# Optimization experiments

Hardware: AMD Instinct MI355X
Metric: run time of the kernel (lower is better)

Reference implementation:

```python
import jax, jax.numpy as jnp
import numpy as np

D_C = 16  # c // 4 with c = 64
BN_EPS = 1e-5


def _block(x, w, b, g, beta, m, v, a):
    """Conv2Dblock with 1x1 conv: pointwise conv -> BatchNorm2d (inference) -> PReLU."""
    y = jnp.einsum('oi,bift->boft', w, x) + b[None, :, None, None]
    scale = (g / jnp.sqrt(v + BN_EPS))[None, :, None, None]
    y = (y - m[None, :, None, None]) * scale + beta[None, :, None, None]
    return jnp.where(y >= 0, y, a * y)  # PReLU, single shared slope


def _asa(inp, fqkv, tqk, proj):
    b, c, f, t = inp.shape
    scale = 1.0 / np.sqrt(D_C)
    neg = -jnp.finfo(inp.dtype).max

    # frequency attention
    f_qkv = _block(inp, *fqkv)                      # [b, 3*d_c interleaved, f, t]
    f_qkv = f_qkv.reshape(b, D_C, 3, f, t)          # '(c k)' split, k fastest
    qf, kf, v = f_qkv[:, :, 0], f_qkv[:, :, 1], f_qkv[:, :, 2]
    f_score = jnp.einsum('bcft,bcyt->btfy', qf, kf) * scale
    f_score = jax.nn.softmax(f_score, axis=-1)
    f_out = jnp.einsum('btfy,bcyt->bcft', f_score, v)

    # causal time attention
    t_qk = _block(inp, *tqk)                        # [b, 2*d_c interleaved, f, t]
    t_qk = t_qk.reshape(b, D_C, 2, f, t)
    qt, kt = t_qk[:, :, 0], t_qk[:, :, 1]
    t_score = jnp.einsum('bcft,bcfy->bfty', qt, kt) * scale
    causal_mask = jnp.triu(jnp.ones((t, t), dtype=bool), 1)  # strictly upper => future
    t_score = jnp.where(causal_mask[None, None], neg, t_score)
    t_score = jax.nn.softmax(t_score, axis=-1)
    t_out = jnp.einsum('bfty,bcfy->bcft', t_score, f_out)

    out = _block(t_out, *proj)
    return out + inp


def setup_inputs() -> dict:
    key = jax.random.key(0)
    ks = jax.random.split(key, 24)
    B, C, F, T = 2, 64, 257, 500
    dc = D_C

    def conv_params(ki, kb, out_ch, in_ch):
        w = jax.random.normal(ki, (out_ch, in_ch), jnp.float32) * (1.0 / np.sqrt(in_ch))
        b = jax.random.normal(kb, (out_ch,), jnp.float32) * 0.02
        return w, b

    inp = jax.random.normal(ks[0], (B, C, F, T), jnp.float32)

    fqkv_w, fqkv_b = conv_params(ks[1], ks[2], 3 * dc, C)
    fqkv_g = 1.0 + 0.1 * jax.random.uniform(ks[3], (3 * dc,), jnp.float32)
    fqkv_beta = 0.02 * jax.random.normal(ks[4], (3 * dc,), jnp.float32)
    fqkv_m = 0.02 * jax.random.normal(ks[5], (3 * dc,), jnp.float32)
    fqkv_v = 0.9 + 0.2 * jax.random.uniform(ks[6], (3 * dc,), jnp.float32)
    fqkv_a = jnp.full((1,), 0.25, jnp.float32)

    tqk_w, tqk_b = conv_params(ks[7], ks[8], 2 * dc, C)
    tqk_g = 1.0 + 0.1 * jax.random.uniform(ks[9], (2 * dc,), jnp.float32)
    tqk_beta = 0.02 * jax.random.normal(ks[10], (2 * dc,), jnp.float32)
    tqk_m = 0.02 * jax.random.normal(ks[11], (2 * dc,), jnp.float32)
    tqk_v = 0.9 + 0.2 * jax.random.uniform(ks[12], (2 * dc,), jnp.float32)
    tqk_a = jnp.full((1,), 0.25, jnp.float32)

    proj_w, proj_b = conv_params(ks[13], ks[14], C, dc)
    proj_g = 1.0 + 0.1 * jax.random.uniform(ks[15], (C,), jnp.float32)
    proj_beta = 0.02 * jax.random.normal(ks[16], (C,), jnp.float32)
    proj_m = 0.02 * jax.random.normal(ks[17], (C,), jnp.float32)
    proj_v = 0.9 + 0.2 * jax.random.uniform(ks[18], (C,), jnp.float32)
    proj_a = jnp.full((1,), 0.25, jnp.float32)

    return dict(inp=inp,
                fqkv_w=fqkv_w, fqkv_b=fqkv_b, fqkv_g=fqkv_g, fqkv_beta=fqkv_beta,
                fqkv_m=fqkv_m, fqkv_v=fqkv_v, fqkv_a=fqkv_a,
                tqk_w=tqk_w, tqk_b=tqk_b, tqk_g=tqk_g, tqk_beta=tqk_beta,
                tqk_m=tqk_m, tqk_v=tqk_v, tqk_a=tqk_a,
                proj_w=proj_w, proj_b=proj_b, proj_g=proj_g, proj_beta=proj_beta,
                proj_m=proj_m, proj_v=proj_v, proj_a=proj_a)


def reference(inp, fqkv_w, fqkv_b, fqkv_g, fqkv_beta, fqkv_m, fqkv_v, fqkv_a,
              tqk_w, tqk_b, tqk_g, tqk_beta, tqk_m, tqk_v, tqk_a,
              proj_w, proj_b, proj_g, proj_beta, proj_m, proj_v, proj_a):
    return _asa(inp,
                (fqkv_w, fqkv_b, fqkv_g, fqkv_beta, fqkv_m, fqkv_v, fqkv_a),
                (tqk_w, tqk_b, tqk_g, tqk_beta, tqk_m, tqk_v, tqk_a),
                (proj_w, proj_b, proj_g, proj_beta, proj_m, proj_v, proj_a))
```

## Files before the change

kernel.cpp:

```cpp
#include <hip/hip_runtime.h>

#define BB 2
#define CIN 64
#define FD 257
#define TD 500
#define FT (FD*TD)
#define EPS 1e-5f
#define NEGINF (-3.0e38f)
#define FDP 260
#define FDP4 260
#define FQT_PLANE (TD*FDP)
#define LOG2E 1.44269504088896f
#define EXP2F(x) __builtin_amdgcn_exp2f(x)

typedef _Float16 half_t;
typedef half_t half2_t __attribute__((ext_vector_type(2)));
typedef half_t half4 __attribute__((ext_vector_type(4)));
typedef float  f32x4 __attribute__((ext_vector_type(4)));

__global__ __launch_bounds__(256) void stage1_kernel(
    const float* __restrict__ x,
    const float* __restrict__ fw, const float* __restrict__ fb_,
    const float* __restrict__ fg, const float* __restrict__ fbe,
    const float* __restrict__ fm, const float* __restrict__ fv_,
    const float* __restrict__ fa,
    const float* __restrict__ tw, const float* __restrict__ tb_,
    const float* __restrict__ tg, const float* __restrict__ tbe,
    const float* __restrict__ tm, const float* __restrict__ tv_,
    const float* __restrict__ ta,
    half_t* __restrict__ fq, half_t* __restrict__ tq)
{
    __shared__ float Wl[80*64];
    __shared__ float Bl[80];
    const int tid = threadIdx.x;
    for (int idx = tid; idx < 80*64; idx += 256) {
        const int o = idx >> 6, i = idx & 63;
        float sc, wv;
        if (o < 48) { sc = fg[o]*rsqrtf(fv_[o]+EPS); wv = fw[o*64+i]; }
        else { const int o2 = o-48; sc = tg[o2]*rsqrtf(tv_[o2]+EPS); wv = tw[o2*64+i]; }
        Wl[idx] = wv*sc;
    }
    if (tid < 80) {
        const int o = tid;
        if (o < 48) Bl[o] = (fb_[o]-fm[o])*(fg[o]*rsqrtf(fv_[o]+EPS)) + fbe[o];
        else { const int o2 = o-48; Bl[o] = (tb_[o2]-tm[o2])*(tg[o2]*rsqrtf(tv_[o2]+EPS)) + tbe[o2]; }
    }
    __syncthreads();
    const float af = fa[0], at = ta[0];
    const int og = tid >> 6, lane = tid & 63;
    const int b  = blockIdx.x / 1004;
    const int nb = blockIdx.x % 1004;
    const long n0 = (long)nb*128 + lane*2;
    if (n0 >= FT) return;

    float2 acc[20];
    #pragma unroll
    for (int j = 0; j < 20; ++j) {
        const float bv = Bl[og*20+j];
        acc[j] = make_float2(bv, bv);
    }
    const float* xb = x + (long)b*CIN*FT + n0;
    #pragma unroll 2
    for (int i = 0; i < 64; i += 4) {
        const float* xi = xb + (long)i*FT;
        const float2 a0 = *(const float2*)(xi);
        const float2 a1 = *(const float2*)(xi + FT);
        const float2 a2 = *(const float2*)(xi + 2*FT);
        const float2 a3 = *(const float2*)(xi + 3*FT);
        #pragma unroll
        for (int j = 0; j < 20; ++j) {
            const float4 wv = *(const float4*)&Wl[(og*20+j)*64 + i];
            acc[j].x += wv.x*a0.x + wv.y*a1.x + wv.z*a2.x + wv.w*a3.x;
            acc[j].y += wv.x*a0.y + wv.y*a1.y + wv.z*a2.y + wv.w*a3.y;
        }
    }
    #pragma unroll
    for (int j = 0; j < 20; ++j) {
        const int o = og*20 + j;
        const float a_ = (o < 48) ? af : at;
        float vx = acc[j].x, vy = acc[j].y;
        vx = vx >= 0.f ? vx : a_*vx;
        vy = vy >= 0.f ? vy : a_*vy;
        half2_t hv; hv[0] = (half_t)vx; hv[1] = (half_t)vy;
        half_t* dst = (o < 48) ? (fq + ((long)b*48 + o)*FT + n0)
                               : (tq + ((long)b*32 + (o-48))*FT + n0);
        *(half2_t*)dst = hv;
    }
}

__global__ __launch_bounds__(256) void transpose_h2h_kernel(
    const half_t* __restrict__ src, half_t* __restrict__ dst,
    int R, int C, int RP)
{
    __shared__ half_t tile[64][68];
    const int plane = blockIdx.x;
    const int rb = blockIdx.y*64, cb = blockIdx.z*64;
    const half_t* s = src + (long)plane*R*C;
    half_t* d = dst + (long)plane*C*RP;
    const int q4 = (threadIdx.x & 15)*4;
    const int wl = threadIdx.x >> 4;
    #pragma unroll
    for (int p = 0; p < 4; ++p) {
        const int r = rb + wl + 16*p;
        const int c = cb + q4;
        half4 v = {(half_t)0.f,(half_t)0.f,(half_t)0.f,(half_t)0.f};
        if (r < R) {
            const half_t* srow = s + (long)r*C;
            if (c + 3 < C) v = *(const half4*)(srow + c);
            else {
                #pragma unroll
                for (int e = 0; e < 4; ++e) if (c+e < C) v[e] = srow[c+e];
            }
        }
        *(half4*)&tile[wl + 16*p][q4] = v;
    }
    __syncthreads();
    #pragma unroll
    for (int p = 0; p < 4; ++p) {
        const int c = cb + wl + 16*p;
        if (c >= C) continue;
        const int r0 = rb + q4;
        half4 o;
        #pragma unroll
        for (int e = 0; e < 4; ++e) o[e] = tile[q4 + e][wl + 16*p];
        half_t* drow = d + (long)c*RP;
        if (r0 + 3 < RP) *(half4*)(drow + r0) = o;
        else {
            #pragma unroll
            for (int e = 0; e < 4; ++e) if (r0+e < RP) drow[r0+e] = o[e];
        }
    }
}

__global__ __launch_bounds__(256) void transpose_f2h_kernel(
    const float* __restrict__ src, half_t* __restrict__ dst,
    int R, int C, int CS, int RP)
{
    __shared__ half_t tile[64][68];
    const int plane = blockIdx.x;
    const int rb = blockIdx.y*64, cb = blockIdx.z*64;
    const float* s = src + (long)plane*R*CS;
    half_t* d = dst + (long)plane*C*RP;
    const int q4 = (threadIdx.x & 15)*4;
    const int wl = threadIdx.x >> 4;
    #pragma unroll
    for (int p = 0; p < 4; ++p) {
        const int r = rb + wl + 16*p;
        const int c = cb + q4;
        half4 v = {(half_t)0.f,(half_t)0.f,(half_t)0.f,(half_t)0.f};
        if (r < R) {
            const float* srow = s + (long)r*CS;
            if (c + 3 < C) {
                const float4 fv = *(const float4*)(srow + c);
                v[0] = (half_t)fv.x; v[1] = (half_t)fv.y;
                v[2] = (half_t)fv.z; v[3] = (half_t)fv.w;
            } else {
                #pragma unroll
                for (int e = 0; e < 4; ++e) if (c+e < C) v[e] = (half_t)srow[c+e];
            }
        }
        *(half4*)&tile[wl + 16*p][q4] = v;
    }
    __syncthreads();
    #pragma unroll
    for (int p = 0; p < 4; ++p) {
        const int c = cb + wl + 16*p;
        if (c >= C) continue;
        const int r0 = rb + q4;
        half4 o;
        #pragma unroll
        for (int e = 0; e < 4; ++e) o[e] = tile[q4 + e][wl + 16*p];
        half_t* drow = d + (long)c*RP;
        if (r0 + 3 < RP) *(half4*)(drow + r0) = o;
        else {
            #pragma unroll
            for (int e = 0; e < 4; ++e) if (r0+e < RP) drow[r0+e] = o[e];
        }
    }
}

__global__ __launch_bounds__(512) void fattn_kernel(
    const half_t* __restrict__ fqT, float* __restrict__ foT)
{
    __shared__ half_t KT[272*20];
    __shared__ half_t QT[272*20];
    __shared__ half_t Vs[16*280];
    const int tid = threadIdx.x;
    const int b = blockIdx.x / TD, t = blockIdx.x % TD;
    const half_t* base = fqT + (long)b*48*FQT_PLANE + (long)t*FDP;
    const half_t qsc = (half_t)(0.25f*LOG2E);
    for (int s = tid; s < 48*68; s += 512) {
        const int c3 = s / 68, j = s - c3*68;
        const int f0 = 4*j;
        half4 v = {(half_t)0.f,(half_t)0.f,(half_t)0.f,(half_t)0.f};
        if (f0 < FDP) v = *(const half4*)(base + (long)c3*FQT_PLANE + f0);
        const int c = c3 / 3, wh = c3 - 3*c;
        if (wh == 0) {
            #pragma unroll
            for (int e = 0; e < 4; ++e) QT[(f0+e)*20 + c] = v[e]*qsc;
        } else if (wh == 1) {
            #pragma unroll
            for (int e = 0; e < 4; ++e) KT[(f0+e)*20 + c] = v[e];
        } else {
            *(half4*)&Vs[c*280 + f0] = v;
        }
    }
    __syncthreads();
    const int w = tid >> 6, lane = tid & 63;
    const int lmod = lane & 15, ldiv = lane >> 4;
    for (int ft = w; ft < 17; ft += 8) {
        const int f0 = 16*ft;
        const half4 qb = *(const half4*)&QT[(f0+lmod)*20 + 4*ldiv];
        f32x4 o = {0.f,0.f,0.f,0.f};
        float m = NEGINF, l = 0.f;
        for (int yt = 0; yt < 16; yt += 2) {
            const int y0 = 16*yt;
            const half4 ka0 = *(const half4*)&KT[(y0   +lmod)*20 + 4*ldiv];
            const half4 ka1 = *(const half4*)&KT[(y0+16+lmod)*20 + 4*ldiv];
            f32x4 s0 = __builtin_amdgcn_mfma_f32_16x16x16f16(
                ka0, qb, (f32x4){0.f,0.f,0.f,0.f}, 0, 0, 0);
            f32x4 s1 = __builtin_amdgcn_mfma_f32_16x16x16f16(
                ka1, qb, (f32x4){0.f,0.f,0.f,0.f}, 0, 0, 0);
            float mt = fmaxf(fmaxf(fmaxf(s0[0],s0[1]), fmaxf(s0[2],s0[3])),
                             fmaxf(fmaxf(s1[0],s1[1]), fmaxf(s1[2],s1[3])));
            mt = fmaxf(mt, __shfl_xor(mt, 16, 64));
            mt = fmaxf(mt, __shfl_xor(mt, 32, 64));
            const float mn = fmaxf(m, mt);
            const float alpha = EXP2F(m - mn);
            half4 pb0, pb1; float ps = 0.f;
            #pragma unroll
            for (int r = 0; r < 4; ++r) {
                const float p0 = EXP2F(s0[r] - mn);
                const float p1 = EXP2F(s1[r] - mn);
                pb0[r] = (half_t)p0; pb1[r] = (half_t)p1;
                ps += p0 + p1;
            }
            ps += __shfl_xor(ps, 16, 64);
            ps += __shfl_xor(ps, 32, 64);
            l = l*alpha + ps;  m = mn;
            o[0] *= alpha; o[1] *= alpha; o[2] *= alpha; o[3] *= alpha;
            const half4 va0 = *(const half4*)&Vs[lmod*280 + y0      + 4*ldiv];
            const half4 va1 = *(const half4*)&Vs[lmod*280 + y0 + 16 + 4*ldiv];
            o = __builtin_amdgcn_mfma_f32_16x16x16f16(va0, pb0, o, 0, 0, 0);
            o = __builtin_amdgcn_mfma_f32_16x16x16f16(va1, pb1, o, 0, 0, 0);
        }
        {
            const int y0 = 256;
            const half4 ka = *(const half4*)&KT[(y0+lmod)*20 + 4*ldiv];
            f32x4 s = __builtin_amdgcn_mfma_f32_16x16x16f16(
                ka, qb, (f32x4){0.f,0.f,0.f,0.f}, 0, 0, 0);
            #pragma unroll
            for (int r = 0; r < 4; ++r)
                if (y0 + 4*ldiv + r >= FD) s[r] = NEGINF;
            float mt = fmaxf(fmaxf(s[0],s[1]), fmaxf(s[2],s[3]));
            mt = fmaxf(mt, __shfl_xor(mt, 16, 64));
            mt = fmaxf(mt, __shfl_xor(mt, 32, 64));
            const float mn = fmaxf(m, mt);
            const float alpha = EXP2F(m - mn);
            half4 pb; float ps = 0.f;
            #pragma unroll
            for (int r = 0; r < 4; ++r) {
                const float p = EXP2F(s[r] - mn);
                pb[r] = (half_t)p; ps += p;
            }
            ps += __shfl_xor(ps, 16, 64);
            ps += __shfl_xor(ps, 32, 64);
            l = l*alpha + ps;  m = mn;
            o[0] *= alpha; o[1] *= alpha; o[2] *= alpha; o[3] *= alpha;
            const half4 va = *(const half4*)&Vs[lmod*280 + y0 + 4*ldiv];
            o = __builtin_amdgcn_mfma_f32_16x16x16f16(va, pb, o, 0, 0, 0);
        }
        const float inv = 1.f/l;
        const int f = f0 + lmod;
        if (f < FD) {
            #pragma unroll
            for (int r = 0; r < 4; ++r) {
                const int c = 4*ldiv + r;
                foT[((long)(b*16 + c)*TD + t)*FDP4 + f] = o[r]*inv;
            }
        }
    }
}

__global__ __launch_bounds__(512) void tattn_kernel(
    const half_t* __restrict__ tq, const half_t* __restrict__ fo,
    float* __restrict__ tout)
{
    extern __shared__ half_t lds[];
    half_t* KT  = lds;
    half_t* QT  = KT + 512*20;
    half_t* FOs = QT + 512*20;
    const int tid = threadIdx.x;
    const int b = blockIdx.x / FD, f = blockIdx.x % FD;
    const half_t* qbase = tq + (long)b*32*FT + (long)f*TD;
    const half_t* fbase = fo + (long)b*16*FT + (long)f*TD;
    const half_t qsc = (half_t)(0.25f*LOG2E);
    for (int idx = tid; idx < 16*128; idx += 512) {
        const int c = idx >> 7, y4 = (idx & 127)*4;
        half4 qv = {(half_t)0.f,(half_t)0.f,(half_t)0.f,(half_t)0.f};
        half4 kv = qv, fv = qv;
        if (y4 + 3 < TD) {
            qv = *(const half4*)(qbase + (long)(2*c  )*FT + y4);
            kv = *(const half4*)(qbase + (long)(2*c+1)*FT + y4);
            fv = *(const half4*)(fbase + (long)c*FT + y4);
        }
        #pragma unroll
        for (int e = 0; e < 4; ++e) {
            QT[(y4+e)*20 + c] = qv[e]*qsc;
            KT[(y4+e)*20 + c] = kv[e];
        }
        *(half4*)&FOs[c*520 + y4] = fv;
    }
    __syncthreads();
    const int w = tid >> 6, lane = tid & 63;
    const int lmod = lane & 15, ldiv = lane >> 4;
    const int tts[4] = {w, 15-w, 16+w, 31-w};
    #pragma unroll
    for (int i = 0; i < 4; ++i) {
        const int tt = tts[i];
        const int t0 = 16*tt;
        const half4 qb = *(const half4*)&QT[(t0+lmod)*20 + 4*ldiv];
        f32x4 o = {0.f,0.f,0.f,0.f};
        float m = NEGINF, l = 0.f;
        int yt = 0;
        for (; yt + 1 < tt; yt += 2) {
            const int y0 = 16*yt;
            const half4 ka0 = *(const half4*)&KT[(y0   +lmod)*20 + 4*ldiv];
            const half4 ka1 = *(const half4*)&KT[(y0+16+lmod)*20 + 4*ldiv];
            f32x4 s0 = __builtin_amdgcn_mfma_f32_16x16x16f16(
                ka0, qb, (f32x4){0.f,0.f,0.f,0.f}, 0, 0, 0);
            f32x4 s1 = __builtin_amdgcn_mfma_f32_16x16x16f16(
                ka1, qb, (f32x4){0.f,0.f,0.f,0.f}, 0, 0, 0);
            float mt = fmaxf(fmaxf(fmaxf(s0[0],s0[1]), fmaxf(s0[2],s0[3])),
                             fmaxf(fmaxf(s1[0],s1[1]), fmaxf(s1[2],s1[3])));
            mt = fmaxf(mt, __shfl_xor(mt, 16, 64));
            mt = fmaxf(mt, __shfl_xor(mt, 32, 64));
            const float mn = fmaxf(m, mt);
            const float alpha = EXP2F(m - mn);
            half4 pb0, pb1; float ps = 0.f;
            #pragma unroll
            for (int r = 0; r < 4; ++r) {
                const float p0 = EXP2F(s0[r] - mn);
                const float p1 = EXP2F(s1[r] - mn);
                pb0[r] = (half_t)p0; pb1[r] = (half_t)p1;
                ps += p0 + p1;
            }
            ps += __shfl_xor(ps, 16, 64);
            ps += __shfl_xor(ps, 32, 64);
            l = l*alpha + ps;  m = mn;
            o[0] *= alpha; o[1] *= alpha; o[2] *= alpha; o[3] *= alpha;
            const half4 fa0 = *(const half4*)&FOs[lmod*520 + y0      + 4*ldiv];
            const half4 fa1 = *(const half4*)&FOs[lmod*520 + y0 + 16 + 4*ldiv];
            o = __builtin_amdgcn_mfma_f32_16x16x16f16(fa0, pb0, o, 0, 0, 0);
            o = __builtin_amdgcn_mfma_f32_16x16x16f16(fa1, pb1, o, 0, 0, 0);
        }
        if (yt < tt) {
            const int y0 = 16*yt;
            const half4 ka0 = *(const half4*)&KT[(y0   +lmod)*20 + 4*ldiv];
            const half4 ka1 = *(const half4*)&KT[(y0+16+lmod)*20 + 4*ldiv];
            f32x4 s0 = __builtin_amdgcn_mfma_f32_16x16x16f16(
                ka0, qb, (f32x4){0.f,0.f,0.f,0.f}, 0, 0, 0);
            f32x4 s1 = __builtin_amdgcn_mfma_f32_16x16x16f16(
                ka1, qb, (f32x4){0.f,0.f,0.f,0.f}, 0, 0, 0);
            #pragma unroll
            for (int r = 0; r < 4; ++r)
                if (4*ldiv + r > lmod) s1[r] = NEGINF;
            float mt = fmaxf(fmaxf(fmaxf(s0[0],s0[1]), fmaxf(s0[2],s0[3])),
                             fmaxf(fmaxf(s1[0],s1[1]), fmaxf(s1[2],s1[3])));
            mt = fmaxf(mt, __shfl_xor(mt, 16, 64));
            mt = fmaxf(mt, __shfl_xor(mt, 32, 64));
            const float mn = fmaxf(m, mt);
            const float alpha = EXP2F(m - mn);
            half4 pb0, pb1; float ps = 0.f;
            #pragma unroll
            for (int r = 0; r < 4; ++r) {
                const float p0 = EXP2F(s0[r] - mn);
                const float p1 = EXP2F(s1[r] - mn);
                pb0[r] = (half_t)p0; pb1[r] = (half_t)p1;
                ps += p0 + p1;
            }
            ps += __shfl_xor(ps, 16, 64);
            ps += __shfl_xor(ps, 32, 64);
            l = l*alpha + ps;  m = mn;
            o[0] *= alpha; o[1] *= alpha; o[2] *= alpha; o[3] *= alpha;
            const half4 fa0 = *(const half4*)&FOs[lmod*520 + y0      + 4*ldiv];
            const half4 fa1 = *(const half4*)&FOs[lmod*520 + y0 + 16 + 4*ldiv];
            o = __builtin_amdgcn_mfma_f32_16x16x16f16(fa0, pb0, o, 0, 0, 0);
            o = __builtin_amdgcn_mfma_f32_16x16x16f16(fa1, pb1, o, 0, 0, 0);
        } else {
            const int y0 = 16*tt;
            const half4 ka = *(const half4*)&KT[(y0+lmod)*20 + 4*ldiv];
            f32x4 s = __builtin_amdgcn_mfma_f32_16x16x16f16(
                ka, qb, (f32x4){0.f,0.f,0.f,0.f}, 0, 0, 0);
            #pragma unroll
            for (int r = 0; r < 4; ++r)
                if (4*ldiv + r > lmod) s[r] = NEGINF;
            float mt = fmaxf(fmaxf(s[0],s[1]), fmaxf(s[2],s[3]));
            mt = fmaxf(mt, __shfl_xor(mt, 16, 64));
            mt = fmaxf(mt, __shfl_xor(mt, 32, 64));
            const float mn = fmaxf(m, mt);
            const float alpha = EXP2F(m - mn);
            half4 pb; float ps = 0.f;
            #pragma unroll
            for (int r = 0; r < 4; ++r) {
                const float p = EXP2F(s[r] - mn);
                pb[r] = (half_t)p; ps += p;
            }
            ps += __shfl_xor(ps, 16, 64);
            ps += __shfl_xor(ps, 32, 64);
            l = l*alpha + ps;  m = mn;
            o[0] *= alpha; o[1] *= alpha; o[2] *= alpha; o[3] *= alpha;
            const half4 fa4 = *(const half4*)&FOs[lmod*520 + y0 + 4*ldiv];
            o = __builtin_amdgcn_mfma_f32_16x16x16f16(fa4, pb, o, 0, 0, 0);
        }
        const float inv = 1.f/l;
        const int t = t0 + lmod;
        if (t < TD) {
            #pragma unroll
            for (int r = 0; r < 4; ++r) {
                const int c = 4*ldiv + r;
                tout[((long)(b*16 + c)*FD + f)*TD + t] = o[r]*inv;
            }
        }
    }
}

__global__ __launch_bounds__(256) void proj_kernel(
    const float* __restrict__ tout, const float* __restrict__ x,
    const float* __restrict__ pw, const float* __restrict__ pb_,
    const float* __restrict__ pg, const float* __restrict__ pbe,
    const float* __restrict__ pm, const float* __restrict__ pv_,
    const float* __restrict__ pa,
    float* __restrict__ out)
{
    __shared__ float PW[64*16];
    __shared__ float PB[64];
    const int tid = threadIdx.x;
    for (int idx = tid; idx < 64*16; idx += 256) {
        const int o = idx >> 4;
        PW[idx] = pw[idx]*(pg[o]*rsqrtf(pv_[o]+EPS));
    }
    if (tid < 64) {
        const int o = tid;
        PB[o] = (pb_[o]-pm[o])*(pg[o]*rsqrtf(pv_[o]+EPS)) + pbe[o];
    }
    __syncthreads();
    const float ap = pa[0];
    const int og = tid >> 6, lane = tid & 63;
    const int b  = blockIdx.x / 1004;
    const int nb = blockIdx.x % 1004;
    const long n0 = (long)nb*128 + lane*2;
    if (n0 >= FT) return;
    float2 acc[16];
    #pragma unroll
    for (int j = 0; j < 16; ++j) {
        const float bv = PB[og*16+j];
        acc[j] = make_float2(bv, bv);
    }
    const float* tb = tout + (long)b*16*FT + n0;
    #pragma unroll
    for (int cc = 0; cc < 16; cc += 4) {
        const float* tc = tb + (long)cc*FT;
        const float2 t0 = *(const float2*)(tc);
        const float2 t1 = *(const float2*)(tc + FT);
        const float2 t2 = *(const float2*)(tc + 2*FT);
        const float2 t3 = *(const float2*)(tc + 3*FT);
        #pragma unroll
        for (int j = 0; j < 16; ++j) {
            const float4 wv = *(const float4*)&PW[(og*16+j)*16 + cc];
            acc[j].x += wv.x*t0.x + wv.y*t1.x + wv.z*t2.x + wv.w*t3.x;
            acc[j].y += wv.x*t0.y + wv.y*t1.y + wv.z*t2.y + wv.w*t3.y;
        }
    }
    #pragma unroll
    for (int j = 0; j < 16; ++j) {
        const int o = og*16 + j;
        float vx = acc[j].x, vy = acc[j].y;
        vx = vx >= 0.f ? vx : ap*vx;
        vy = vy >= 0.f ? vy : ap*vy;
        const long gi = (long)(b*64 + o)*FT + n0;
        const float2 xv = *(const float2*)(x + gi);
        float2 v; v.x = vx + xv.x; v.y = vy + xv.y;
        *(float2*)(out + gi) = v;
    }
}

extern "C" void kernel_launch(void* const* d_in, const int* in_sizes, int n_in,
                              void* d_out, int out_size, void* d_ws, size_t ws_size,
                              hipStream_t stream)
{
    const float* x     = (const float*)d_in[0];
    const float* fw    = (const float*)d_in[1];
    const float* fb_   = (const float*)d_in[2];
    const float* fg    = (const float*)d_in[3];
    const float* fbe   = (const float*)d_in[4];
    const float* fm    = (const float*)d_in[5];
    const float* fv_   = (const float*)d_in[6];
    const float* fa    = (const float*)d_in[7];
    const float* tw    = (const float*)d_in[8];
    const float* tb_   = (const float*)d_in[9];
    const float* tg    = (const float*)d_in[10];
    const float* tbe   = (const float*)d_in[11];
    const float* tm    = (const float*)d_in[12];
    const float* tv_   = (const float*)d_in[13];
    const float* ta    = (const float*)d_in[14];
    const float* pw    = (const float*)d_in[15];
    const float* pb_   = (const float*)d_in[16];
    const float* pg    = (const float*)d_in[17];
    const float* pbe   = (const float*)d_in[18];
    const float* pm    = (const float*)d_in[19];
    const float* pv_   = (const float*)d_in[20];
    const float* pa    = (const float*)d_in[21];
    float* out = (float*)d_out;

    char* base = (char*)d_ws;
    const size_t szA = (size_t)BB*48*FT*sizeof(half_t);
    const size_t szB = (size_t)BB*16*FT*sizeof(half_t);
    const size_t szC = (size_t)BB*32*FT*sizeof(half_t);
    const size_t szD = (size_t)96*FQT_PLANE*sizeof(half_t);
    const size_t need = szA + szB + szC + szD;
    if (ws_size < need) return;
    half_t* fqh  = (half_t*)base;
    float*  foT  = (float*)base;
    half_t* foh  = (half_t*)(base + szA);
    half_t* tqh  = (half_t*)(base + szA + szB);
    half_t* fqTh = (half_t*)(base + szA + szB + szC);
    float*  tout = (float*)(base + szA + szB + szC);

    stage1_kernel<<<dim3(BB*1004), dim3(256), 0, stream>>>(
        x, fw, fb_, fg, fbe, fm, fv_, fa, tw, tb_, tg, tbe, tm, tv_, ta, fqh, tqh);

    transpose_h2h_kernel<<<dim3(BB*48, 5, 8), dim3(256), 0, stream>>>(
        fqh, fqTh, FD, TD, FDP);

    fattn_kernel<<<dim3(BB*TD), dim3(512), 0, stream>>>(fqTh, foT);

    transpose_f2h_kernel<<<dim3(BB*16, 8, 5), dim3(256), 0, stream>>>(
        foT, foh, TD, FD, FDP4, TD);

    const int tlds = (512*20*2 + 16*520)*(int)sizeof(half_t);
    (void)hipFuncSetAttribute(reinterpret_cast<const void*>(tattn_kernel),
                        hipFuncAttributeMaxDynamicSharedMemorySize, tlds);
    tattn_kernel<<<dim3(BB*FD), dim3(512), tlds, stream>>>(tqh, foh, tout);

    proj_kernel<<<dim3(BB*1004), dim3(256), 0, stream>>>(
        tout, x, pw, pb_, pg, pbe, pm, pv_, pa, out);
}
```

Baseline: 325.0 us.

## Use fp16 MFMA for input pointwise conv; split proj channels across blocks

Stage1's 80x64 pointwise conv moves from scalar fp32 FMAs onto 16x16x16 fp16 MFMA instructions. Weights are stored in LDS as fp16 and x is converted to fp16 per lane, which lowers conv input precision and switches to scalar strided loads and 2-byte stores. proj_kernel now splits the 64 output channels into two 32-channel halves across block pairs and processes 4 points per thread with float4 loads and stores, which reads tout twice but lowers register pressure.

```diff
diff --git a/kernel.cpp b/kernel.cpp
--- a/kernel.cpp
+++ b/kernel.cpp
@@ -30,15 +30,15 @@
     const float* __restrict__ ta,
     half_t* __restrict__ fq, half_t* __restrict__ tq)
 {
-    __shared__ float Wl[80*64];
-    __shared__ float Bl[80];
+    __shared__ half_t Wh[80][68];
+    __shared__ float  Bl[80];
     const int tid = threadIdx.x;
     for (int idx = tid; idx < 80*64; idx += 256) {
         const int o = idx >> 6, i = idx & 63;
         float sc, wv;
         if (o < 48) { sc = fg[o]*rsqrtf(fv_[o]+EPS); wv = fw[o*64+i]; }
         else { const int o2 = o-48; sc = tg[o2]*rsqrtf(tv_[o2]+EPS); wv = tw[o2*64+i]; }
-        Wl[idx] = wv*sc;
+        Wh[o][i] = (half_t)(wv*sc);
     }
     if (tid < 80) {
         const int o = tid;
@@ -47,44 +47,61 @@
     }
     __syncthreads();
     const float af = fa[0], at = ta[0];
-    const int og = tid >> 6, lane = tid & 63;
+    const int w = tid >> 6, lane = tid & 63;
+    const int lmod = lane & 15, ldiv = lane >> 4;
     const int b  = blockIdx.x / 1004;
     const int nb = blockIdx.x % 1004;
-    const long n0 = (long)nb*128 + lane*2;
-    if (n0 >= FT) return;
-
-    float2 acc[20];
-    #pragma unroll
-    for (int j = 0; j < 20; ++j) {
-        const float bv = Bl[og*20+j];
-        acc[j] = make_float2(bv, bv);
-    }
-    const float* xb = x + (long)b*CIN*FT + n0;
-    #pragma unroll 2
-    for (int i = 0; i < 64; i += 4) {
-        const float* xi = xb + (long)i*FT;
-        const float2 a0 = *(const float2*)(xi);
-        const float2 a1 = *(const float2*)(xi + FT);
-        const float2 a2 = *(const float2*)(xi + 2*FT);
-        const float2 a3 = *(const float2*)(xi + 3*FT);
-        #pragma unroll
-        for (int j = 0; j < 20; ++j) {
-            const float4 wv = *(const float4*)&Wl[(og*20+j)*64 + i];
-            acc[j].x += wv.x*a0.x + wv.y*a1.x + wv.z*a2.x + wv.w*a3.x;
-            acc[j].y += wv.x*a0.y + wv.y*a1.y + wv.z*a2.y + wv.w*a3.y;
-        }
-    }
-    #pragma unroll
-    for (int j = 0; j < 20; ++j) {
-        const int o = og*20 + j;
-        const float a_ = (o < 48) ? af : at;
-        float vx = acc[j].x, vy = acc[j].y;
-        vx = vx >= 0.f ? vx : a_*vx;
-        vy = vy >= 0.f ? vy : a_*vy;
-        half2_t hv; hv[0] = (half_t)vx; hv[1] = (half_t)vy;
-        half_t* dst = (o < 48) ? (fq + ((long)b*48 + o)*FT + n0)
-                               : (tq + ((long)b*32 + (o-48))*FT + n0);
-        *(half2_t*)dst = hv;
+    const long n0 = (long)nb*128;
+
+    half4 a[5][4];
+    #pragma unroll
+    for (int ot = 0; ot < 5; ++ot)
+        #pragma unroll
+        for (int ks = 0; ks < 4; ++ks)
+            a[ot][ks] = *(const half4*)&Wh[16*ot + lmod][16*ks + 4*ldiv];
+    f32x4 bias[5];
+    #pragma unroll
+    for (int ot = 0; ot < 5; ++ot)
+        #pragma unroll
+        for (int r = 0; r < 4; ++r)
+            bias[ot][r] = Bl[16*ot + 4*ldiv + r];
+
+    const float* xplane = x + (long)b*CIN*FT;
+    #pragma unroll
+    for (int pt = 0; pt < 2; ++pt) {
+        const long p = n0 + 32*w + 16*pt + lmod;
+        const bool ok = p < FT;
+        const long pc = ok ? p : 0;
+        const float* xp = xplane + pc;
+        half4 bfr[4];
+        #pragma unroll
+        for (int ks = 0; ks < 4; ++ks) {
+            #pragma unroll
+            for (int e = 0; e < 4; ++e) {
+                const int ch = 16*ks + 4*ldiv + e;
+                bfr[ks][e] = (half_t)xp[(long)ch*FT];
+            }
+        }
+        #pragma unroll
+        for (int ot = 0; ot < 5; ++ot) {
+            f32x4 acc = bias[ot];
+            #pragma unroll
+            for (int ks = 0; ks < 4; ++ks)
+                acc = __builtin_amdgcn_mfma_f32_16x16x16f16(a[ot][ks], bfr[ks], acc, 0, 0, 0);
+            const float alpha = (ot < 3) ? af : at;
+            if (ok) {
+                #pragma unroll
+                for (int r = 0; r < 4; ++r) {
+                    const int o = 16*ot + 4*ldiv + r;
+                    float v = acc[r];
+                    v = v >= 0.f ? v : alpha*v;
+                    half_t hv = (half_t)v;
+                    half_t* dst = (o < 48) ? (fq + ((long)b*48 + o)*FT + p)
+                                           : (tq + ((long)b*32 + (o-48))*FT + p);
+                    dst[0] = hv;
+                }
+            }
+        }
     }
 }
 
@@ -433,55 +450,62 @@
     const float* __restrict__ pa,
     float* __restrict__ out)
 {
-    __shared__ float PW[64*16];
-    __shared__ float PB[64];
+    __shared__ float PW[32*16];
+    __shared__ float PB[32];
     const int tid = threadIdx.x;
-    for (int idx = tid; idx < 64*16; idx += 256) {
-        const int o = idx >> 4;
-        PW[idx] = pw[idx]*(pg[o]*rsqrtf(pv_[o]+EPS));
-    }
-    if (tid < 64) {
-        const int o = tid;
-        PB[o] = (pb_[o]-pm[o])*(pg[o]*rsqrtf(pv_[o]+EPS)) + pbe[o];
+    const int cg   = blockIdx.x & 1;
+    const int bidx = blockIdx.x >> 1;
+    const int ob   = cg*32;
+    for (int idx = tid; idx < 32*16; idx += 256) {
+        const int ol = idx >> 4;
+        const int o = ob + ol;
+        PW[idx] = pw[o*16 + (idx & 15)]*(pg[o]*rsqrtf(pv_[o]+EPS));
+    }
+    if (tid < 32) {
+        const int o = ob + tid;
+        PB[tid] = (pb_[o]-pm[o])*(pg[o]*rsqrtf(pv_[o]+EPS)) + pbe[o];
     }
     __syncthreads();
     const float ap = pa[0];
     const int og = tid >> 6, lane = tid & 63;
-    const int b  = blockIdx.x / 1004;
-    const int nb = blockIdx.x % 1004;
-    const long n0 = (long)nb*128 + lane*2;
+    const int b  = bidx / 502;
+    const int nb = bidx % 502;
+    const long n0 = (long)nb*256 + lane*4;
     if (n0 >= FT) return;
-    float2 acc[16];
-    #pragma unroll
-    for (int j = 0; j < 16; ++j) {
-        const float bv = PB[og*16+j];
-        acc[j] = make_float2(bv, bv);
+    float4 acc[8];
+    #pragma unroll
+    for (int j = 0; j < 8; ++j) {
+        const float bv = PB[og*8+j];
+        acc[j] = make_float4(bv, bv, bv, bv);
     }
     const float* tb = tout + (long)b*16*FT + n0;
-    #pragma unroll
     for (int cc = 0; cc < 16; cc += 4) {
         const float* tc = tb + (long)cc*FT;
-        const float2 t0 = *(const float2*)(tc);
-        const float2 t1 = *(const float2*)(tc + FT);
-        const float2 t2 = *(const float2*)(tc + 2*FT);
-        const float2 t3 = *(const float2*)(tc + 3*FT);
-        #pragma unroll
-        for (int j = 0; j < 16; ++j) {
-            const float4 wv = *(const float4*)&PW[(og*16+j)*16 + cc];
+        const float4 t0 = *(const float4*)(tc);
+        const float4 t1 = *(const float4*)(tc + FT);
+        const float4 t2 = *(const float4*)(tc + 2*FT);
+        const float4 t3 = *(const float4*)(tc + 3*FT);
+        #pragma unroll
+        for (int j = 0; j < 8; ++j) {
+            const float4 wv = *(const float4*)&PW[(og*8+j)*16 + cc];
             acc[j].x += wv.x*t0.x + wv.y*t1.x + wv.z*t2.x + wv.w*t3.x;
             acc[j].y += wv.x*t0.y + wv.y*t1.y + wv.z*t2.y + wv.w*t3.y;
-        }
-    }
-    #pragma unroll
-    for (int j = 0; j < 16; ++j) {
-        const int o = og*16 + j;
-        float vx = acc[j].x, vy = acc[j].y;
-        vx = vx >= 0.f ? vx : ap*vx;
-        vy = vy >= 0.f ? vy : ap*vy;
+            acc[j].z += wv.x*t0.z + wv.y*t1.z + wv.z*t2.z + wv.w*t3.z;
+            acc[j].w += wv.x*t0.w + wv.y*t1.w + wv.z*t2.w + wv.w*t3.w;
+        }
+    }
+    #pragma unroll
+    for (int j = 0; j < 8; ++j) {
+        const int o = ob + og*8 + j;
+        float4 v = acc[j];
+        v.x = v.x >= 0.f ? v.x : ap*v.x;
+        v.y = v.y >= 0.f ? v.y : ap*v.y;
+        v.z = v.z >= 0.f ? v.z : ap*v.z;
+        v.w = v.w >= 0.f ? v.w : ap*v.w;
         const long gi = (long)(b*64 + o)*FT + n0;
-        const float2 xv = *(const float2*)(x + gi);
-        float2 v; v.x = vx + xv.x; v.y = vy + xv.y;
-        *(float2*)(out + gi) = v;
+        const float4 xv = *(const float4*)(x + gi);
+        v.x += xv.x; v.y += xv.y; v.z += xv.z; v.w += xv.w;
+        *(float4*)(out + gi) = v;
     }
 }
 
@@ -543,6 +567,6 @@
                         hipFuncAttributeMaxDynamicSharedMemorySize, tlds);
     tattn_kernel<<<dim3(BB*FD), dim3(512), tlds, stream>>>(tqh, foh, tout);
 
-    proj_kernel<<<dim3(BB*1004), dim3(256), 0, stream>>>(
+    proj_kernel<<<dim3(BB*502*2), dim3(256), 0, stream>>>(
         tout, x, pw, pb_, pg, pbe, pm, pv_, pa, out);
 }
```

Measured after the change: 293.0 us. -9.8%, faster.
